# Performance work log

Measured on AMD Instinct MI355X. Metric: run time of the kernel, lower is better.

Reference implementation:

```python
import jax, jax.numpy as jnp
import numpy as np

B = 256          # batchSize
KNEG = 4096      # K negatives
D = 128          # inputSize
N = 1000000      # outputSize (memory bank rows)
T = 0.07
MOM = 0.5
STDV = 1.0 / np.sqrt(D / 3.0)


def setup_inputs() -> dict:
    key = jax.random.key(0)
    k1, k2, k3, k4, k5, k6 = jax.random.split(key, 6)
    ab = jax.random.normal(k1, (B, D), dtype=jnp.float32)
    l = jax.random.normal(k2, (B, D), dtype=jnp.float32)
    ss = jax.random.normal(k3, (B, D), dtype=jnp.float32)
    # memory bank initialized uniform in [-stdv, stdv] like the torch buffer
    memory_ab = jax.random.uniform(k4, (N, D), dtype=jnp.float32) * (2 * STDV) - STDV
    idx = jax.random.randint(k5, (B, KNEG + 1), 0, N)
    y = jax.random.randint(k6, (B,), 0, N)
    idx = idx.at[:, 0].set(y)  # positive sample in column 0
    return {"ab": ab, "l": l, "ss": ss, "memory_ab": memory_ab,
            "idx": idx, "y": y}


def reference(ab, l, ss, memory_ab, idx, y):
    # gather: [B, K+1, D]; detached in the original (no grad to the bank)
    w = jax.lax.stop_gradient(memory_ab[idx])
    # three batched dot-product scores against the same gathered weights
    out_l = jnp.einsum('bkd,bd->bk', w, l)[..., None] / T
    out_ss = jnp.einsum('bkd,bd->bk', w, ss)[..., None] / T
    out_orig = jnp.einsum('bkd,bd->bk', w, ab)[..., None] / T
    out = jnp.stack([out_orig, out_l, out_ss])  # [3, B, K+1, 1]
    # momentum scatter-update of the memory bank (no_grad in original)
    ab_pos = memory_ab[y] * MOM + ab * (1.0 - MOM)
    ab_norm = jnp.sqrt(jnp.sum(ab_pos * ab_pos, axis=1, keepdims=True))
    new_memory_ab = jax.lax.stop_gradient(memory_ab.at[y].set(ab_pos / ab_norm))
    return out, new_memory_ab
```

## Files before the change

### kernel.cpp

```cpp
#include <hip/hip_runtime.h>
#include <math.h>

constexpr int Bc   = 256;
constexpr int KP1  = 4097;
constexpr int Dc   = 128;
constexpr int NROW = 1000000;
constexpr float MOM = 0.5f;
constexpr float Tc  = 0.07f;

__global__ __launch_bounds__(256) void copy_mem_kernel(const float4* __restrict__ src,
                                                       float4* __restrict__ dst,
                                                       int n4) {
    int i = blockIdx.x * 256 + threadIdx.x;
    const int stride = gridDim.x * 256;
    for (; i < n4; i += stride) dst[i] = src[i];
}

__global__ __launch_bounds__(64) void scatter_kernel(const float* __restrict__ memory,
                                                     const float* __restrict__ ab,
                                                     const int* __restrict__ y,
                                                     float* __restrict__ out_mem) {
    const int b = blockIdx.x;
    const int row = y[b];
    for (int b2 = b + 1; b2 < Bc; ++b2)
        if (y[b2] == row) return;

    const int lane = threadIdx.x;
    float2 m = *(const float2*)(memory + (size_t)row * Dc + lane * 2);
    float2 a = *(const float2*)(ab + b * Dc + lane * 2);
    float v0 = m.x * MOM + a.x * (1.0f - MOM);
    float v1 = m.y * MOM + a.y * (1.0f - MOM);
    float s = v0 * v0 + v1 * v1;
#pragma unroll
    for (int off = 32; off; off >>= 1) s += __shfl_xor(s, off);
    const float inv = 1.0f / sqrtf(s);
    float2 o;
    o.x = v0 * inv;
    o.y = v1 * inv;
    *(float2*)(out_mem + (size_t)row * Dc + lane * 2) = o;
}

__global__ __launch_bounds__(256) void gather_dot_kernel(
    const float* __restrict__ memory,
    const float* __restrict__ ab,
    const float* __restrict__ l,
    const float* __restrict__ ss,
    const int* __restrict__ idx,
    float* __restrict__ out) {
    const int b    = blockIdx.x;
    const int lane = threadIdx.x & 63;
    const int wid  = (threadIdx.x >> 6) + (blockIdx.y << 2);
    const int nw   = gridDim.y << 2;
    const int g    = lane >> 3;
    const int sub  = lane & 7;

    float4 qa[4], ql[4], qs[4];
#pragma unroll
    for (int it = 0; it < 4; ++it) {
        const int d = it * 32 + sub * 4;
        qa[it] = *(const float4*)(ab + b * Dc + d);
        ql[it] = *(const float4*)(l + b * Dc + d);
        qs[it] = *(const float4*)(ss + b * Dc + d);
    }
    const int* idxb = idx + (size_t)b * KP1;
    const size_t out_b = (size_t)b * KP1;
    const size_t plane = (size_t)Bc * KP1;

    for (int k0 = wid * 8; k0 < KP1; k0 += nw * 8) {
        const int k = k0 + g;
        const int kc = (k < KP1) ? k : (KP1 - 1);
        const int row = idxb[kc];
        const float* wrow = memory + (size_t)row * Dc;
        float sa = 0.f, sl = 0.f, s2 = 0.f;
#pragma unroll
        for (int it = 0; it < 4; ++it) {
            const float4 w = *(const float4*)(wrow + it * 32 + sub * 4);
            sa += w.x * qa[it].x + w.y * qa[it].y + w.z * qa[it].z + w.w * qa[it].w;
            sl += w.x * ql[it].x + w.y * ql[it].y + w.z * ql[it].z + w.w * ql[it].w;
            s2 += w.x * qs[it].x + w.y * qs[it].y + w.z * qs[it].z + w.w * qs[it].w;
        }
#pragma unroll
        for (int off = 1; off < 8; off <<= 1) {
            sa += __shfl_xor(sa, off);
            sl += __shfl_xor(sl, off);
            s2 += __shfl_xor(s2, off);
        }
        if (sub == 0 && k < KP1) {
            out[0 * plane + out_b + k] = sa / Tc;
            out[1 * plane + out_b + k] = sl / Tc;
            out[2 * plane + out_b + k] = s2 / Tc;
        }
    }
}

extern "C" void kernel_launch(void* const* d_in, const int* in_sizes, int n_in,
                              void* d_out, int out_size, void* d_ws, size_t ws_size,
                              hipStream_t stream) {
    const float* ab     = (const float*)d_in[0];
    const float* l      = (const float*)d_in[1];
    const float* ss     = (const float*)d_in[2];
    const float* memory = (const float*)d_in[3];
    const int*   idx    = (const int*)d_in[4];
    const int*   y      = (const int*)d_in[5];

    float* out     = (float*)d_out;
    float* out_mem = out + (size_t)3 * Bc * KP1;

    const int n4 = (NROW * Dc) / 4;
    copy_mem_kernel<<<dim3(2048), dim3(256), 0, stream>>>(
        (const float4*)memory, (float4*)out_mem, n4);
    scatter_kernel<<<dim3(Bc), dim3(64), 0, stream>>>(memory, ab, y, out_mem);
    gather_dot_kernel<<<dim3(Bc, 16), dim3(256), 0, stream>>>(memory, ab, l, ss, idx, out);
}
```

Baseline: 313.6 us.

## Unroll bank copy with nontemporal stores and prefetch gather indices

The memory-bank copy kernel now issues four independent vector loads per thread before writing them back with nontemporal stores, and its grid doubles. The gather-dot kernel uses twice as many blocks in y, preloads all of its row indices into registers in a fully unrolled loop so the gathers can overlap, and multiplies by 1/T instead of dividing. The aim is more memory-level parallelism on the 512 MB copy and the random gather, and less cache pollution from the streamed output. The costs are higher register use and a slightly different rounding from the reciprocal multiply.

Measured after the change: 303.9 us, median of 2. -3.1%, faster.

```diff
diff --git a/kernel.cpp b/kernel.cpp
--- a/kernel.cpp
+++ b/kernel.cpp
@@ -8,12 +8,24 @@
 constexpr float MOM = 0.5f;
 constexpr float Tc  = 0.07f;
 
-__global__ __launch_bounds__(256) void copy_mem_kernel(const float4* __restrict__ src,
-                                                       float4* __restrict__ dst,
+typedef float f4 __attribute__((ext_vector_type(4)));
+
+__global__ __launch_bounds__(256) void copy_mem_kernel(const f4* __restrict__ src,
+                                                       f4* __restrict__ dst,
                                                        int n4) {
     int i = blockIdx.x * 256 + threadIdx.x;
-    const int stride = gridDim.x * 256;
-    for (; i < n4; i += stride) dst[i] = src[i];
+    const int S = gridDim.x * 256;
+    for (; i + 3 * S < n4; i += 4 * S) {
+        f4 a0 = src[i];
+        f4 a1 = src[i + S];
+        f4 a2 = src[i + 2 * S];
+        f4 a3 = src[i + 3 * S];
+        __builtin_nontemporal_store(a0, &dst[i]);
+        __builtin_nontemporal_store(a1, &dst[i + S]);
+        __builtin_nontemporal_store(a2, &dst[i + 2 * S]);
+        __builtin_nontemporal_store(a3, &dst[i + 3 * S]);
+    }
+    for (; i < n4; i += S) __builtin_nontemporal_store(src[i], &dst[i]);
 }
 
 __global__ __launch_bounds__(64) void scatter_kernel(const float* __restrict__ memory,
@@ -40,6 +52,11 @@
     *(float2*)(out_mem + (size_t)row * Dc + lane * 2) = o;
 }
 
+constexpr int GY    = 32;
+constexpr int NW    = GY * 4;
+constexpr int KSTEP = NW * 8;
+constexpr int NITER = (KP1 + KSTEP - 1) / KSTEP;
+
 __global__ __launch_bounds__(256) void gather_dot_kernel(
     const float* __restrict__ memory,
     const float* __restrict__ ab,
@@ -50,7 +67,6 @@
     const int b    = blockIdx.x;
     const int lane = threadIdx.x & 63;
     const int wid  = (threadIdx.x >> 6) + (blockIdx.y << 2);
-    const int nw   = gridDim.y << 2;
     const int g    = lane >> 3;
     const int sub  = lane & 7;
 
@@ -59,18 +75,26 @@
     for (int it = 0; it < 4; ++it) {
         const int d = it * 32 + sub * 4;
         qa[it] = *(const float4*)(ab + b * Dc + d);
-        ql[it] = *(const float4*)(l + b * Dc + d);
+        ql[it] = *(const float4*)(l  + b * Dc + d);
         qs[it] = *(const float4*)(ss + b * Dc + d);
     }
     const int* idxb = idx + (size_t)b * KP1;
     const size_t out_b = (size_t)b * KP1;
     const size_t plane = (size_t)Bc * KP1;
+    const float invT = 1.0f / Tc;
+    const int kbase = wid * 8 + g;
 
-    for (int k0 = wid * 8; k0 < KP1; k0 += nw * 8) {
-        const int k = k0 + g;
-        const int kc = (k < KP1) ? k : (KP1 - 1);
-        const int row = idxb[kc];
-        const float* wrow = memory + (size_t)row * Dc;
+    int rows[NITER];
+#pragma unroll
+    for (int t = 0; t < NITER; ++t) {
+        int k = kbase + t * KSTEP;
+        rows[t] = idxb[(k < KP1) ? k : (KP1 - 1)];
+    }
+
+#pragma unroll
+    for (int t = 0; t < NITER; ++t) {
+        const int k = kbase + t * KSTEP;
+        const float* wrow = memory + (size_t)rows[t] * Dc;
         float sa = 0.f, sl = 0.f, s2 = 0.f;
 #pragma unroll
         for (int it = 0; it < 4; ++it) {
@@ -86,9 +110,9 @@
             s2 += __shfl_xor(s2, off);
         }
         if (sub == 0 && k < KP1) {
-            out[0 * plane + out_b + k] = sa / Tc;
-            out[1 * plane + out_b + k] = sl / Tc;
-            out[2 * plane + out_b + k] = s2 / Tc;
+            out[0 * plane + out_b + k] = sa * invT;
+            out[1 * plane + out_b + k] = sl * invT;
+            out[2 * plane + out_b + k] = s2 * invT;
         }
     }
 }
@@ -107,8 +131,8 @@
     float* out_mem = out + (size_t)3 * Bc * KP1;
 
     const int n4 = (NROW * Dc) / 4;
-    copy_mem_kernel<<<dim3(2048), dim3(256), 0, stream>>>(
-        (const float4*)memory, (float4*)out_mem, n4);
+    copy_mem_kernel<<<dim3(4096), dim3(256), 0, stream>>>(
+        (const f4*)memory, (f4*)out_mem, n4);
     scatter_kernel<<<dim3(Bc), dim3(64), 0, stream>>>(memory, ab, y, out_mem);
-    gather_dot_kernel<<<dim3(Bc, 16), dim3(256), 0, stream>>>(memory, ab, l, ss, idx, out);
+    gather_dot_kernel<<<dim3(Bc, GY), dim3(256), 0, stream>>>(memory, ab, l, ss, idx, out);
 }
```
